# Kernel optimization log

Hardware: AMD Instinct MI355X
Metric: run time of the kernel (lower is better)

Reference implementation:

```python
import jax, jax.numpy as jnp
import numpy as np

S = 256          # fine grid extent (active region within full_scale=4096)
SC = S // 2      # coarse grid extent after stride-2 downsample
N = 400_000      # active fine voxels
C_IN, M0, M1 = 3, 32, 64   # input features; unet_structure = [32, 64]
NCLASS = 20
EPS = 1e-4       # scn.BatchNormReLU default eps


def _build_nbr(keys_sorted, coords, s):
    """27-neighborhood index table for a sparse voxel set (hash via sorted keys)."""
    n = coords.shape[0]
    nbr = np.full((n, 27), -1, dtype=np.int32)
    x, y, z = coords[:, 0], coords[:, 1], coords[:, 2]
    k = 0
    for dx in (-1, 0, 1):
        for dy in (-1, 0, 1):
            for dz in (-1, 0, 1):
                nx, ny, nz = x + dx, y + dy, z + dz
                valid = (nx >= 0) & (nx < s) & (ny >= 0) & (ny < s) & (nz >= 0) & (nz < s)
                ck = (nx.astype(np.int64) * s + ny) * s + nz
                pos = np.clip(np.searchsorted(keys_sorted, ck), 0, n - 1)
                nbr[:, k] = np.where(valid & (keys_sorted[pos] == ck), pos, -1)
                k += 1
    return nbr


def setup_inputs() -> dict:
    rng = np.random.default_rng(0)
    keys = np.sort(rng.choice(S ** 3, size=N, replace=False).astype(np.int64))
    x = keys // (S * S); y = (keys // S) % S; z = keys % S
    coords = np.stack([x, y, z], 1)
    nbr_fine = _build_nbr(keys, coords, S)
    # stride-2 pooling structure
    ckeys = ((x // 2) * SC + (y // 2)) * SC + (z // 2)
    uk, parent_id = np.unique(ckeys, return_inverse=True)
    ccoords = np.stack([uk // (SC * SC), (uk // SC) % SC, uk % SC], 1)
    nbr_coarse = _build_nbr(uk, ccoords, SC)
    child_off = ((x & 1) * 4 + (y & 1) * 2 + (z & 1)).astype(np.int32)

    ks = jax.random.split(jax.random.key(0), 16)
    def w(k, shape, fan_in):
        return jax.random.normal(k, shape, jnp.float32) * (1.0 / np.sqrt(fan_in))
    return {
        "feats": jax.random.normal(ks[0], (N, C_IN), jnp.float32),
        "nbr_fine": jnp.asarray(nbr_fine),
        "nbr_coarse": jnp.asarray(nbr_coarse),
        "parent_id": jnp.asarray(parent_id.astype(np.int32)),
        "child_off": jnp.asarray(child_off),
        "W_sub": w(ks[1], (27, C_IN, M0), 27 * C_IN),
        "W_e0": w(ks[2], (27, M0, M0), 27 * M0),
        "g0": jnp.ones((M0,), jnp.float32), "b0": jnp.zeros((M0,), jnp.float32),
        "W_down": w(ks[3], (8, M0, M1), 8 * M0),
        "W_e1": w(ks[4], (27, M1, M1), 27 * M1),
        "g1": jnp.ones((M1,), jnp.float32), "b1": jnp.zeros((M1,), jnp.float32),
        "W_up": w(ks[5], (8, M1, M0), 8 * M1),
        "W_dec": w(ks[6], (27, 2 * M0, M0), 27 * 2 * M0),
        "g_out": jnp.ones((M0,), jnp.float32), "b_out": jnp.zeros((M0,), jnp.float32),
        "W_lin": w(ks[7], (M0, NCLASS), M0),
        "b_lin": jnp.zeros((NCLASS,), jnp.float32),
    }


def _subconv(feat, nbr, W):
    """Submanifold 3x3x3 conv: fixed loop over 27 kernel taps (gather+GEMM)."""
    out = jnp.zeros((feat.shape[0], W.shape[2]), feat.dtype)
    for k in range(27):
        idx = nbr[:, k]
        g = jnp.where(idx[:, None] >= 0, feat[jnp.clip(idx, 0)], 0.0)
        out = out + g @ W[k]
    return out


def _bnrelu(xv, g, b):
    mu = xv.mean(0)
    var = xv.var(0)
    return jax.nn.relu((xv - mu) * jax.lax.rsqrt(var + EPS) * g + b)


def reference(feats, nbr_fine, nbr_coarse, parent_id, child_off,
              W_sub, W_e0, g0, b0, W_down, W_e1, g1, b1, W_up, W_dec,
              g_out, b_out, W_lin, b_lin):
    M = nbr_coarse.shape[0]
    xv = _subconv(feats, nbr_fine, W_sub)                       # [N, M0]
    e0 = _bnrelu(_subconv(xv, nbr_fine, W_e0), g0, b0)          # encoder level 0
    # stride-2 sparse conv (scatter-add children into parents, per-offset weight)
    down = jax.ops.segment_sum(jnp.einsum('nc,ncd->nd', e0, W_down[child_off]),
                               parent_id, num_segments=M)        # [M, M1]
    e1 = _bnrelu(_subconv(down, nbr_coarse, W_e1), g1, b1)      # encoder level 1
    # stride-2 sparse deconv (gather parent, per-offset weight)
    up = jnp.einsum('nc,ncd->nd', e1[parent_id], W_up[child_off])  # [N, M0]
    dec = _subconv(jnp.concatenate([e0, up], 1), nbr_fine, W_dec)  # decoder join
    feature = _bnrelu(dec, g_out, b_out)                        # final BatchNormReLU
    y = feature @ W_lin + b_lin                                 # class head
    return (y, feature)
```

## Files before the change

kernel.cpp:

```cpp
#include <hip/hip_runtime.h>
#include <hip/hip_bf16.h>

#define BN_EPS 1e-4f

typedef __attribute__((ext_vector_type(8))) short short8;
typedef __attribute__((ext_vector_type(4))) float float4e;

__device__ __forceinline__ int rfl(int x) { return __builtin_amdgcn_readfirstlane(x); }

__device__ __forceinline__ float ldf(const __hip_bfloat16* p) { return __bfloat162float(*p); }
__device__ __forceinline__ void stf(__hip_bfloat16* p, float v) { *p = __float2bfloat16(v); }

__device__ __forceinline__ short bfbits(float x) {
    __hip_bfloat16 h = __float2bfloat16(x);
    short s;
    __builtin_memcpy(&s, &h, 2);
    return s;
}
__device__ __forceinline__ short8 cvt8(float4 a, float4 b) {
    short8 r;
    r[0] = bfbits(a.x); r[1] = bfbits(a.y); r[2] = bfbits(a.z); r[3] = bfbits(a.w);
    r[4] = bfbits(b.x); r[5] = bfbits(b.y); r[6] = bfbits(b.z); r[7] = bfbits(b.w);
    return r;
}

__global__ __launch_bounds__(256) void k_pack(const float* __restrict__ src,
                                              __hip_bfloat16* __restrict__ dst,
                                              int CIN, int COUT, int KT, int NT, int total) {
    int i = blockIdx.x * 256 + threadIdx.x;
    if (i >= total) return;
    int j = i & 7, lane = (i >> 3) & 63;
    int g = i >> 9;
    int nt = g % NT; g /= NT;
    int kt = g % KT; g /= KT;
    int t = g;
    int q = lane >> 4, c = lane & 15;
    dst[i] = __float2bfloat16(src[((size_t)t * CIN + kt * 32 + q * 8 + j) * COUT + nt * 16 + c]);
}

__global__ __launch_bounds__(256) void k_xv(const float* __restrict__ feats,
                                            const int* __restrict__ nbr,
                                            const float* __restrict__ W,
                                            __hip_bfloat16* __restrict__ out, int N) {
    int n = blockIdx.x * 256 + threadIdx.x;
    if (n >= N) return;
    float acc[32];
#pragma unroll
    for (int d = 0; d < 32; ++d) acc[d] = 0.f;
    const int* nb = nbr + (size_t)n * 27;
    int idx[27];
#pragma unroll
    for (int k = 0; k < 27; ++k) idx[k] = nb[k];
#pragma unroll
    for (int g = 0; g < 3; ++g) {
        float fx[9], fy[9], fz[9];
#pragma unroll
        for (int j = 0; j < 9; ++j) {
            int id = idx[g * 9 + j];
            size_t c = (size_t)(id < 0 ? 0 : id);
            const float* p = feats + c * 3;
            fx[j] = p[0]; fy[j] = p[1]; fz[j] = p[2];
        }
#pragma unroll
        for (int j = 0; j < 9; ++j) {
            int k = g * 9 + j;
            float m = idx[k] >= 0 ? 1.f : 0.f;
            float f0 = fx[j] * m, f1 = fy[j] * m, f2 = fz[j] * m;
            const float* w = W + k * 96;
#pragma unroll
            for (int d = 0; d < 32; ++d)
                acc[d] += f0 * w[d] + f1 * w[32 + d] + f2 * w[64 + d];
        }
    }
    short8* o = (short8*)(out + (size_t)n * 32);
#pragma unroll
    for (int c = 0; c < 4; ++c) {
        short8 r;
#pragma unroll
        for (int j = 0; j < 8; ++j) r[j] = bfbits(acc[c * 8 + j]);
        o[c] = r;
    }
}

template <int CIN, int COUT, int MODE, int MAP, int COMPACT>
__global__ __launch_bounds__(256, 4) void k_conv(const void* __restrict__ inAv,
                                                 const void* __restrict__ inBv,
                                                 const int* __restrict__ nbr,
                                                 const __hip_bfloat16* __restrict__ Wp,
                                                 __hip_bfloat16* __restrict__ out,
                                                 int nrows,
                                                 float* __restrict__ ssum,
                                                 float* __restrict__ ssq) {
    constexpr int KT = CIN / 32;
    constexpr int NT = COUT / 16;
    static_assert(KT == 1 || KT == 2, "KT must be 1 or 2");
    static_assert(!(COMPACT == 1 && MODE == 1), "compact path is bf16-only");
    __shared__ int sidx[4][432];
    __shared__ int slist[4][32];
    const __hip_bfloat16* inAb = (const __hip_bfloat16*)inAv;
    const __hip_bfloat16* inBb = (const __hip_bfloat16*)inBv;
    const float* inAf = (const float*)inAv;
    const int tid = threadIdx.x;
    const int lane = tid & 63;
    const int wv = tid >> 6;
    const int m15 = lane & 15;
    const int q = lane >> 4;
    int* my = sidx[wv];
    int* lst = slist[wv];
    const int ntile = (nrows + 15) / 16;
    const int b = blockIdx.x;
    int start, tend, tstep;
    if constexpr (MAP == 0) {
        const int bs = (b & 7) * (gridDim.x >> 3) + (b >> 3);
        const int w = bs * 4 + wv;
        const int nw = gridDim.x * 4;
        const int cq = ntile / nw, cr = ntile % nw;
        start = w * cq + (w < cr ? w : cr);
        tend = start + cq + (w < cr ? 1 : 0);
        tstep = 1;
    } else {
        const int xcd = b & 7;
        const int wpx = (gridDim.x >> 3) * 4;
        const int lw = (b >> 3) * 4 + wv;
        const int s0 = (int)(((long long)xcd * ntile) >> 3);
        const int s1 = (int)(((long long)(xcd + 1) * ntile) >> 3);
        start = s0 + lw;
        tend = s1;
        tstep = wpx;
    }
    float sS[NT], sQ[NT];
#pragma unroll
    for (int nt = 0; nt < NT; ++nt) { sS[nt] = 0.f; sQ[nt] = 0.f; }

    const short8 z8 = (short8)(short)0;

    for (int tile = start; tile < tend; tile += tstep) {
        const int row0 = rfl(tile) * 16;
        int nr = nrows - row0;
        nr = nr > 16 ? 16 : nr;
        const int* src = nbr + (size_t)row0 * 27;
        const int tot = nr * 27;
        float4e acc[NT];
#pragma unroll
        for (int nt = 0; nt < NT; ++nt) acc[nt] = (float4e)0.f;

        if constexpr (COMPACT) {
            unsigned ab = 0;
            for (int t = lane; t < 432; t += 64) {
                int v = (t < tot) ? src[t] : -1;
                my[t] = v;
                if (v >= 0) ab |= (1u << (t % 27));
            }
#pragma unroll
            for (int s = 1; s < 64; s <<= 1) ab |= __shfl_xor((int)ab, s);
            {
                bool act = (lane < 27) && ((ab >> lane) & 1u);
                unsigned long long bal = __ballot(act);
                if (act) lst[__popcll(bal & ((1ull << lane) - 1ull))] = lane;
            }
            const int nact = __popc((int)ab);

            auto load_s = [&](int ir, short8& s0_, short8& s1_) {
                size_t id = (size_t)(ir < 0 ? 0 : ir);
                if constexpr (MODE == 0) {
                    s0_ = *(const short8*)(inAb + id * CIN + q * 8);
                    if constexpr (KT == 2)
                        s1_ = *(const short8*)(inAb + id * CIN + 32 + q * 8);
                } else {
                    s0_ = *(const short8*)(inAb + id * 32 + q * 8);
                    s1_ = *(const short8*)(inBb + id * 32 + q * 8);
                }
            };
            auto mfma_s = [&](int ktap, int irv, short8 a0, short8 a1) {
                a0 = (irv >= 0) ? a0 : z8;
                if constexpr (KT == 2) a1 = (irv >= 0) ? a1 : z8;
                const short8* bp = (const short8*)Wp + (size_t)ktap * (KT * NT * 64) + lane;
#pragma unroll
                for (int nt = 0; nt < NT; ++nt) {
                    acc[nt] = __builtin_amdgcn_mfma_f32_16x16x32_bf16(a0, bp[nt * 64], acc[nt], 0, 0, 0);
                    if constexpr (KT == 2)
                        acc[nt] = __builtin_amdgcn_mfma_f32_16x16x32_bf16(a1, bp[(NT + nt) * 64], acc[nt], 0, 0, 0);
                }
            };

            short8 sX0 = z8, sX1 = z8, sY0 = z8, sY1 = z8, sZ0 = z8, sZ1 = z8;
            int kX = 0, kY = 0, kZ = 0, irX = -1, irY = -1, irZ = -1;
            if (0 < nact) { kX = lst[0]; irX = my[m15 * 27 + kX]; load_s(irX, sX0, sX1); }
            if (1 < nact) { kY = lst[1]; irY = my[m15 * 27 + kY]; load_s(irY, sY0, sY1); }
            if (2 < nact) { kZ = lst[2]; irZ = my[m15 * 27 + kZ]; load_s(irZ, sZ0, sZ1); }
            int i = 0;
            while (i < nact) {
                mfma_s(kX, irX, sX0, sX1);
                if (i + 3 < nact) { kX = lst[i + 3]; irX = my[m15 * 27 + kX]; load_s(irX, sX0, sX1); }
                if (++i >= nact) break;
                mfma_s(kY, irY, sY0, sY1);
                if (i + 3 < nact) { kY = lst[i + 3]; irY = my[m15 * 27 + kY]; load_s(irY, sY0, sY1); }
                if (++i >= nact) break;
                mfma_s(kZ, irZ, sZ0, sZ1);
                if (i + 3 < nact) { kZ = lst[i + 3]; irZ = my[m15 * 27 + kZ]; load_s(irZ, sZ0, sZ1); }
                ++i;
            }
        } else {
            for (int t = lane; t < 432; t += 64) my[t] = (t < tot) ? src[t] : -1;

            short8 sA0 = z8, sA1 = z8, sB0 = z8, sB1 = z8, sC0 = z8, sC1 = z8;
            float4 fA0{}, fA1{}, fA2{}, fA3{};
            float4 fB0{}, fB1{}, fB2{}, fB3{};
            float4 fC0{}, fC1{}, fC2{}, fC3{};

            auto load_g = [&](int ir, short8& s0_, short8& s1_,
                              float4& f0, float4& f1, float4& f2, float4& f3) {
                size_t id = (size_t)(ir < 0 ? 0 : ir);
                if constexpr (MODE == 0) {
                    s0_ = *(const short8*)(inAb + id * CIN + q * 8);
                    if constexpr (KT == 2)
                        s1_ = *(const short8*)(inAb + id * CIN + 32 + q * 8);
                } else if constexpr (MODE == 2) {
                    s0_ = *(const short8*)(inAb + id * 32 + q * 8);
                    s1_ = *(const short8*)(inBb + id * 32 + q * 8);
                } else {
                    const float* bb = inAf + id * 64 + q * 8;
                    f0 = *(const float4*)(bb);
                    f1 = *(const float4*)(bb + 4);
                    f2 = *(const float4*)(bb + 32);
                    f3 = *(const float4*)(bb + 36);
                }
            };

            int irA = my[m15 * 27 + 0];
            int irB = my[m15 * 27 + 1];
            int irC = my[m15 * 27 + 2];
            int mA = rfl((int)(__ballot(irA >= 0) & 0xffff));
            int mB = rfl((int)(__ballot(irB >= 0) & 0xffff));
            if (mA) load_g(irA, sA0, sA1, fA0, fA1, fA2, fA3);
            if (mB) load_g(irB, sB0, sB1, fB0, fB1, fB2, fB3);
            for (int k = 0; k < 27; ++k) {
                int mC = rfl((int)(__ballot(irC >= 0) & 0xffff));
                int irD = -1;
                if (k + 3 < 27) irD = my[m15 * 27 + (k + 3)];
                if (mC) load_g(irC, sC0, sC1, fC0, fC1, fC2, fC3);
                if (mA) {
                    short8 a0, a1;
                    if constexpr (MODE == 1) {
                        a0 = cvt8(fA0, fA1);
                        a1 = cvt8(fA2, fA3);
                    } else {
                        a0 = sA0;
                        a1 = sA1;
                    }
                    a0 = (irA >= 0) ? a0 : z8;
                    if constexpr (KT == 2) a1 = (irA >= 0) ? a1 : z8;
                    const short8* bp = (const short8*)Wp + (size_t)k * KT * NT * 64 + lane;
#pragma unroll
                    for (int nt = 0; nt < NT; ++nt) {
                        acc[nt] = __builtin_amdgcn_mfma_f32_16x16x32_bf16(a0, bp[nt * 64], acc[nt], 0, 0, 0);
                        if constexpr (KT == 2)
                            acc[nt] = __builtin_amdgcn_mfma_f32_16x16x32_bf16(a1, bp[(NT + nt) * 64], acc[nt], 0, 0, 0);
                    }
                }
                mA = mB; mB = mC;
                irA = irB; irB = irC; irC = irD;
                if constexpr (MODE == 1) {
                    fA0 = fB0; fA1 = fB1; fA2 = fB2; fA3 = fB3;
                    fB0 = fC0; fB1 = fC1; fB2 = fC2; fB3 = fC3;
                } else {
                    sA0 = sB0; sB0 = sC0;
                    if constexpr (KT == 2) { sA1 = sB1; sB1 = sC1; }
                }
            }
        }
#pragma unroll
        for (int nt = 0; nt < NT; ++nt) {
#pragma unroll
            for (int r = 0; r < 4; ++r) {
                int rowg = row0 + q * 4 + r;
                if (rowg < nrows) {
                    float v = acc[nt][r];
                    stf(out + (size_t)rowg * COUT + nt * 16 + m15, v);
                    sS[nt] += v;
                    sQ[nt] += v * v;
                }
            }
        }
    }
#pragma unroll
    for (int nt = 0; nt < NT; ++nt) {
        float v = sS[nt], w2 = sQ[nt];
        v += __shfl_xor(v, 16); v += __shfl_xor(v, 32);
        w2 += __shfl_xor(w2, 16); w2 += __shfl_xor(w2, 32);
        if (lane < 16) {
            atomicAdd(&ssum[nt * 16 + lane], v);
            atomicAdd(&ssq[nt * 16 + lane], w2);
        }
    }
}

__global__ void k_fin(const float* __restrict__ ssum, const float* __restrict__ ssq,
                      const float* __restrict__ g, const float* __restrict__ b,
                      float* __restrict__ scale, float* __restrict__ shift,
                      int C, float invN) {
    int c = blockIdx.x * blockDim.x + threadIdx.x;
    if (c >= C) return;
    float mu = ssum[c] * invN;
    float var = fmaxf(ssq[c] * invN - mu * mu, 0.f);
    float s = g[c] * rsqrtf(var + BN_EPS);
    scale[c] = s;
    shift[c] = b[c] - mu * s;
}

__global__ __launch_bounds__(256) void k_down(__hip_bfloat16* __restrict__ e0,
                                              const int* __restrict__ parent,
                                              const int* __restrict__ child,
                                              const float* __restrict__ Wd,
                                              const float* __restrict__ sc,
                                              const float* __restrict__ sh,
                                              float* __restrict__ down, int N) {
    const int lane = threadIdx.x & 63;
    int wid = blockIdx.x * 4 + (threadIdx.x >> 6);
    int nw = gridDim.x * 4;
    for (int row = wid; row < N; row += nw) {
        int urow = rfl(row);
        float v = 0.f;
        if (lane < 32) {
            float r = ldf(e0 + (size_t)urow * 32 + lane);
            v = fmaxf(fmaf(r, sc[lane], sh[lane]), 0.f);
            stf(e0 + (size_t)urow * 32 + lane, v);
        }
        int par = rfl(parent[urow]);
        int off = rfl(child[urow]);
        float acc = 0.f;
        const float* wb = Wd + (size_t)off * 2048 + lane;
#pragma unroll
        for (int c = 0; c < 32; ++c)
            acc = fmaf(__shfl(v, c), wb[c * 64], acc);
        atomicAdd(&down[(size_t)par * 64 + lane], acc);
    }
}

__global__ __launch_bounds__(256) void k_up(const __hip_bfloat16* __restrict__ e1raw,
                                            const int* __restrict__ parent,
                                            const int* __restrict__ child,
                                            const float* __restrict__ Wu,
                                            const float* __restrict__ sc,
                                            const float* __restrict__ sh,
                                            __hip_bfloat16* __restrict__ up, int N) {
    const int lane = threadIdx.x & 63;
    int wid = blockIdx.x * 4 + (threadIdx.x >> 6);
    int nw = gridDim.x * 4;
    for (int row = wid; row < N; row += nw) {
        int urow = rfl(row);
        int par = rfl(parent[urow]);
        int off = rfl(child[urow]);
        float e = ldf(e1raw + (size_t)par * 64 + lane);
        float v = fmaxf(fmaf(e, sc[lane], sh[lane]), 0.f);
        int d = lane & 31, hi = lane >> 5;
        float acc = 0.f;
        const float* wb = Wu + (size_t)off * 2048 + (size_t)hi * 1024 + d;
#pragma unroll
        for (int c = 0; c < 32; ++c)
            acc = fmaf(__shfl(v, hi * 32 + c), wb[c * 32], acc);
        acc += __shfl_xor(acc, 32);
        if (hi == 0) stf(up + (size_t)urow * 32 + d, acc);
    }
}

__global__ __launch_bounds__(256) void k_out(const __hip_bfloat16* __restrict__ dec,
                                             const float* __restrict__ sc,
                                             const float* __restrict__ sh,
                                             const float* __restrict__ Wl,
                                             const float* __restrict__ bl,
                                             float* __restrict__ y,
                                             float* __restrict__ feat, int N) {
    int n = blockIdx.x * 256 + threadIdx.x;
    if (n >= N) return;
    float f[32];
    const __hip_bfloat162* p = (const __hip_bfloat162*)(dec + (size_t)n * 32);
#pragma unroll
    for (int j = 0; j < 16; ++j) {
        float2 t = __bfloat1622float2(p[j]);
        f[2 * j + 0] = fmaxf(fmaf(t.x, sc[2 * j + 0], sh[2 * j + 0]), 0.f);
        f[2 * j + 1] = fmaxf(fmaf(t.y, sc[2 * j + 1], sh[2 * j + 1]), 0.f);
    }
    float4* fo = (float4*)(feat + (size_t)n * 32);
#pragma unroll
    for (int j = 0; j < 8; ++j)
        fo[j] = make_float4(f[4 * j], f[4 * j + 1], f[4 * j + 2], f[4 * j + 3]);
    float acc[20];
#pragma unroll
    for (int qq = 0; qq < 20; ++qq) acc[qq] = bl[qq];
#pragma unroll
    for (int c = 0; c < 32; ++c) {
        float fc = f[c];
#pragma unroll
        for (int qq = 0; qq < 20; ++qq) acc[qq] = fmaf(fc, Wl[c * 20 + qq], acc[qq]);
    }
    float4* yo = (float4*)(y + (size_t)n * 20);
#pragma unroll
    for (int j = 0; j < 5; ++j)
        yo[j] = make_float4(acc[4 * j], acc[4 * j + 1], acc[4 * j + 2], acc[4 * j + 3]);
}

extern "C" void kernel_launch(void* const* d_in, const int* in_sizes, int n_in,
                              void* d_out, int out_size, void* d_ws, size_t ws_size,
                              hipStream_t stream) {
    const float* feats = (const float*)d_in[0];
    const int* nbr_f   = (const int*)d_in[1];
    const int* nbr_c   = (const int*)d_in[2];
    const int* parent  = (const int*)d_in[3];
    const int* child   = (const int*)d_in[4];
    const float* W_sub = (const float*)d_in[5];
    const float* W_e0  = (const float*)d_in[6];
    const float* g0    = (const float*)d_in[7];
    const float* b0    = (const float*)d_in[8];
    const float* W_dn  = (const float*)d_in[9];
    const float* W_e1  = (const float*)d_in[10];
    const float* g1    = (const float*)d_in[11];
    const float* b1    = (const float*)d_in[12];
    const float* W_up  = (const float*)d_in[13];
    const float* W_dec = (const float*)d_in[14];
    const float* g_o   = (const float*)d_in[15];
    const float* b_o   = (const float*)d_in[16];
    const float* W_lin = (const float*)d_in[17];
    const float* b_lin = (const float*)d_in[18];

    const int N = in_sizes[0] / 3;
    const int M = in_sizes[2] / 27;

    float* wsf = (float*)d_ws;
    size_t R = (size_t)M * 64;
    if ((size_t)N * 32 > R) R = (size_t)N * 32;
    __hip_bfloat16* xvb = (__hip_bfloat16*)wsf;
    float* down = wsf;
    __hip_bfloat16* up     = (__hip_bfloat16*)wsf;
    __hip_bfloat16* decraw = (__hip_bfloat16*)(wsf + (size_t)N * 16);
    float* stats = wsf + R;

    __hip_bfloat16* e0    = (__hip_bfloat16*)d_out;
    __hip_bfloat16* e1raw = (__hip_bfloat16*)((float*)d_out + (size_t)N * 16);
    __hip_bfloat16* Wp0   = (__hip_bfloat16*)((float*)d_out + (size_t)N * 16 + (size_t)M * 32);
    const int T0 = 27 * 1 * 2 * 512;
    const int T1 = 27 * 2 * 4 * 512;
    const int T2 = 27 * 2 * 2 * 512;
    __hip_bfloat16* Wp1 = Wp0 + T0;
    __hip_bfloat16* Wp2 = Wp1 + T1;
    float* y    = (float*)d_out;
    float* feat = y + (size_t)N * 20;

    const int nblk = (N + 255) / 256;
    const int G = 2048;

    hipMemsetAsync(stats, 0, 256 * sizeof(float), stream);
    k_pack<<<(T0 + 255) / 256, 256, 0, stream>>>(W_e0, Wp0, 32, 32, 1, 2, T0);
    k_pack<<<(T1 + 255) / 256, 256, 0, stream>>>(W_e1, Wp1, 64, 64, 2, 4, T1);
    k_pack<<<(T2 + 255) / 256, 256, 0, stream>>>(W_dec, Wp2, 64, 32, 2, 2, T2);

    k_xv<<<nblk, 256, 0, stream>>>(feats, nbr_f, W_sub, xvb, N);
    k_conv<32, 32, 0, 1, 1><<<G, 256, 0, stream>>>(xvb, nullptr, nbr_f, Wp0, e0, N,
                                                   stats + 0, stats + 32);
    hipMemsetAsync(down, 0, (size_t)M * 64 * sizeof(float), stream);
    k_fin<<<1, 64, 0, stream>>>(stats + 0, stats + 32, g0, b0,
                                stats + 256, stats + 288, 32, 1.f / (float)N);
    k_down<<<G, 256, 0, stream>>>(e0, parent, child, W_dn,
                                  stats + 256, stats + 288, down, N);
    k_conv<64, 64, 1, 0, 0><<<G, 256, 0, stream>>>(down, nullptr, nbr_c, Wp1, e1raw, M,
                                                   stats + 64, stats + 128);
    k_fin<<<1, 64, 0, stream>>>(stats + 64, stats + 128, g1, b1,
                                stats + 320, stats + 384, 64, 1.f / (float)M);
    k_up<<<G, 256, 0, stream>>>(e1raw, parent, child, W_up,
                                stats + 320, stats + 384, up, N);
    k_conv<64, 32, 2, 1, 1><<<G, 256, 0, stream>>>(e0, up, nbr_f, Wp2, decraw, N,
                                                   stats + 192, stats + 224);
    k_fin<<<1, 64, 0, stream>>>(stats + 192, stats + 224, g_o, b_o,
                                stats + 448, stats + 480, 32, 1.f / (float)N);
    k_out<<<nblk, 256, 0, stream>>>(decraw, stats + 448, stats + 480, W_lin, b_lin,
                                    y, feat, N);
}
```

Measured before the change: 1.398 ms.

## Split coarse conv into two bf16 half-channel passes with fp32 partial accumulation

```diff
diff --git a/kernel.cpp b/kernel.cpp
--- a/kernel.cpp
+++ b/kernel.cpp
@@ -82,7 +82,21 @@
     }
 }
 
-template <int CIN, int COUT, int MODE, int MAP, int COMPACT>
+__global__ __launch_bounds__(256) void k_cvt2(const float* __restrict__ src,
+                                              __hip_bfloat16* __restrict__ lo,
+                                              __hip_bfloat16* __restrict__ hi, int M) {
+    int i = blockIdx.x * 256 + threadIdx.x;
+    if (i >= M * 8) return;
+    int row = i >> 3;
+    int c8 = i & 7;
+    const float4* p = (const float4*)(src + (size_t)row * 64 + c8 * 8);
+    float4 a = p[0], b = p[1];
+    __hip_bfloat16* dst = (c8 < 4) ? (lo + (size_t)row * 32 + c8 * 8)
+                                   : (hi + (size_t)row * 32 + (c8 - 4) * 8);
+    *(short8*)dst = cvt8(a, b);
+}
+
+template <int CIN, int COUT, int MODE, int MAP, int COMPACT, int STORE = 0, int BKT = CIN / 32>
 __global__ __launch_bounds__(256, 4) void k_conv(const void* __restrict__ inAv,
                                                  const void* __restrict__ inBv,
                                                  const int* __restrict__ nbr,
@@ -90,7 +104,8 @@
                                                  __hip_bfloat16* __restrict__ out,
                                                  int nrows,
                                                  float* __restrict__ ssum,
-                                                 float* __restrict__ ssq) {
+                                                 float* __restrict__ ssq,
+                                                 float* __restrict__ part) {
     constexpr int KT = CIN / 32;
     constexpr int NT = COUT / 16;
     static_assert(KT == 1 || KT == 2, "KT must be 1 or 2");
@@ -174,7 +189,7 @@
             auto mfma_s = [&](int ktap, int irv, short8 a0, short8 a1) {
                 a0 = (irv >= 0) ? a0 : z8;
                 if constexpr (KT == 2) a1 = (irv >= 0) ? a1 : z8;
-                const short8* bp = (const short8*)Wp + (size_t)ktap * (KT * NT * 64) + lane;
+                const short8* bp = (const short8*)Wp + (size_t)ktap * (BKT * NT * 64) + lane;
 #pragma unroll
                 for (int nt = 0; nt < NT; ++nt) {
                     acc[nt] = __builtin_amdgcn_mfma_f32_16x16x32_bf16(a0, bp[nt * 64], acc[nt], 0, 0, 0);
@@ -250,7 +265,7 @@
                     }
                     a0 = (irA >= 0) ? a0 : z8;
                     if constexpr (KT == 2) a1 = (irA >= 0) ? a1 : z8;
-                    const short8* bp = (const short8*)Wp + (size_t)k * KT * NT * 64 + lane;
+                    const short8* bp = (const short8*)Wp + (size_t)k * (BKT * NT * 64) + lane;
 #pragma unroll
                     for (int nt = 0; nt < NT; ++nt) {
                         acc[nt] = __builtin_amdgcn_mfma_f32_16x16x32_bf16(a0, bp[nt * 64], acc[nt], 0, 0, 0);
@@ -276,21 +291,29 @@
                 int rowg = row0 + q * 4 + r;
                 if (rowg < nrows) {
                     float v = acc[nt][r];
-                    stf(out + (size_t)rowg * COUT + nt * 16 + m15, v);
-                    sS[nt] += v;
-                    sQ[nt] += v * v;
+                    if constexpr (STORE == 1) {
+                        part[(size_t)rowg * COUT + nt * 16 + m15] = v;
+                    } else {
+                        if constexpr (STORE == 2)
+                            v += part[(size_t)rowg * COUT + nt * 16 + m15];
+                        stf(out + (size_t)rowg * COUT + nt * 16 + m15, v);
+                        sS[nt] += v;
+                        sQ[nt] += v * v;
+                    }
                 }
             }
         }
     }
-#pragma unroll
-    for (int nt = 0; nt < NT; ++nt) {
-        float v = sS[nt], w2 = sQ[nt];
-        v += __shfl_xor(v, 16); v += __shfl_xor(v, 32);
-        w2 += __shfl_xor(w2, 16); w2 += __shfl_xor(w2, 32);
-        if (lane < 16) {
-            atomicAdd(&ssum[nt * 16 + lane], v);
-            atomicAdd(&ssq[nt * 16 + lane], w2);
+    if constexpr (STORE != 1) {
+#pragma unroll
+        for (int nt = 0; nt < NT; ++nt) {
+            float v = sS[nt], w2 = sQ[nt];
+            v += __shfl_xor(v, 16); v += __shfl_xor(v, 32);
+            w2 += __shfl_xor(w2, 16); w2 += __shfl_xor(w2, 32);
+            if (lane < 16) {
+                atomicAdd(&ssum[nt * 16 + lane], v);
+                atomicAdd(&ssq[nt * 16 + lane], w2);
+            }
         }
     }
 }
@@ -456,20 +479,35 @@
 
     k_xv<<<nblk, 256, 0, stream>>>(feats, nbr_f, W_sub, xvb, N);
     k_conv<32, 32, 0, 1, 1><<<G, 256, 0, stream>>>(xvb, nullptr, nbr_f, Wp0, e0, N,
-                                                   stats + 0, stats + 32);
+                                                   stats + 0, stats + 32, nullptr);
     hipMemsetAsync(down, 0, (size_t)M * 64 * sizeof(float), stream);
     k_fin<<<1, 64, 0, stream>>>(stats + 0, stats + 32, g0, b0,
                                 stats + 256, stats + 288, 32, 1.f / (float)N);
     k_down<<<G, 256, 0, stream>>>(e0, parent, child, W_dn,
                                   stats + 256, stats + 288, down, N);
-    k_conv<64, 64, 1, 0, 0><<<G, 256, 0, stream>>>(down, nullptr, nbr_c, Wp1, e1raw, M,
-                                                   stats + 64, stats + 128);
+    {
+        size_t base = (R + 512) * sizeof(float);
+        size_t needb = base + (size_t)M * 64 * sizeof(__hip_bfloat16);
+        if (ws_size >= needb) {
+            __hip_bfloat16* dlo = (__hip_bfloat16*)((char*)d_ws + base);
+            __hip_bfloat16* dhi = dlo + (size_t)M * 32;
+            k_cvt2<<<((M * 8) + 255) / 256, 256, 0, stream>>>(down, dlo, dhi, M);
+            float* part = down;
+            k_conv<32, 64, 0, 0, 0, 1, 2><<<G, 256, 0, stream>>>(
+                dlo, nullptr, nbr_c, Wp1, nullptr, M, nullptr, nullptr, part);
+            k_conv<32, 64, 0, 0, 0, 2, 2><<<G, 256, 0, stream>>>(
+                dhi, nullptr, nbr_c, Wp1 + 2048, e1raw, M, stats + 64, stats + 128, part);
+        } else {
+            k_conv<64, 64, 1, 0, 0, 0, 2><<<G, 256, 0, stream>>>(
+                down, nullptr, nbr_c, Wp1, e1raw, M, stats + 64, stats + 128, nullptr);
+        }
+    }
     k_fin<<<1, 64, 0, stream>>>(stats + 64, stats + 128, g1, b1,
                                 stats + 320, stats + 384, 64, 1.f / (float)M);
     k_up<<<G, 256, 0, stream>>>(e1raw, parent, child, W_up,
                                 stats + 320, stats + 384, up, N);
     k_conv<64, 32, 2, 1, 1><<<G, 256, 0, stream>>>(e0, up, nbr_f, Wp2, decraw, N,
-                                                   stats + 192, stats + 224);
+                                                   stats + 192, stats + 224, nullptr);
     k_fin<<<1, 64, 0, stream>>>(stats + 192, stats + 224, g_o, b_o,
                                 stats + 448, stats + 480, 32, 1.f / (float)N);
     k_out<<<nblk, 256, 0, stream>>>(decraw, stats + 448, stats + 480, W_lin, b_lin,
```

Result: slower. 2.035 ms (+45.5%).
